# Kernel tuning notes

Measured on AMD Instinct MI355X. Metric: run time of the kernel, lower is better.

Reference implementation:

```python
import jax, jax.numpy as jnp
import numpy as np

NUM_HEADS = 8


def setup_inputs() -> dict:
    key = jax.random.key(0)
    ks = jax.random.split(key, 5)
    B, N, D = 2, 2048, 512
    scale = 1.0 / np.sqrt(D)  # xavier-ish init for stability
    return {
        "x": jax.random.normal(ks[0], (B, N, D), dtype=jnp.float32),
        "Wq": jax.random.normal(ks[1], (D, D), dtype=jnp.float32) * scale,
        "Wk": jax.random.normal(ks[2], (D, D), dtype=jnp.float32) * scale,
        "Wv": jax.random.normal(ks[3], (D, D), dtype=jnp.float32) * scale,
        "Wo": jax.random.normal(ks[4], (D, D), dtype=jnp.float32) * scale,
        "log_c": jnp.zeros((), dtype=jnp.float32),
        "log_beta": jnp.zeros((), dtype=jnp.float32),
    }


def reference(x, Wq, Wk, Wv, Wo, log_c, log_beta):
    B, N, D = x.shape
    H = NUM_HEADS
    dh = D // H

    # torch nn.Linear: y = x @ W.T
    def proj(W):
        return (x @ W.T).reshape(B, N, H, dh).transpose(0, 2, 1, 3)  # [B,H,N,dh]

    q, k, v = proj(Wq), proj(Wk), proj(Wv)

    c = jax.nn.softplus(log_c)
    beta = jax.nn.softplus(log_beta) + 0.5

    q_nsq = jnp.sum(q * q, axis=-1)  # [B,H,N]
    k_nsq = jnp.sum(k * k, axis=-1)  # [B,H,N]
    qk = jnp.einsum("bhnd,bhmd->bhnm", q, k)  # [B,H,N,N]

    diff_sq = jnp.maximum(q_nsq[..., :, None] - 2.0 * qk + k_nsq[..., None, :], 0.0)
    hyp_factor = jnp.sqrt(1.0 + c * (q_nsq[..., :, None] + k_nsq[..., None, :]))
    dist = jnp.sqrt(diff_sq + 1e-8) * hyp_factor
    scores = -beta * dist

    # causal mask (original: causal = mask is not None)
    causal = jnp.tril(jnp.ones((N, N), dtype=bool))
    scores = jnp.where(causal, scores, -jnp.inf)

    p = jax.nn.softmax(scores, axis=-1)
    out = jnp.einsum("bhnm,bhmd->bhnd", p, v)  # [B,H,N,dh]
    out = out.transpose(0, 2, 1, 3).reshape(B, N, D)
    return out @ Wo.T
```

## Files before the change

### kernel.cpp

```cpp
#include <hip/hip_runtime.h>
#include <math.h>

#define BB   2
#define NN   2048
#define DDIM 512
#define HH   8
#define DH   64
#define MTOT (BB*NN)
#define EE   (BB*HH*NN*DH)
#define CPB  144
#define NSLOT (BB*HH*CPB)

typedef __attribute__((ext_vector_type(8))) short bf16x8;
typedef __attribute__((ext_vector_type(4))) float f32x4;

__device__ __forceinline__ float softplus_f(float x) {
    return x > 20.f ? x : log1pf(expf(x));
}
__device__ __forceinline__ unsigned short f2bf(float x) {
    union { float f; unsigned u; } v; v.f = x;
    unsigned r = v.u + 0x7fffu + ((v.u >> 16) & 1u);
    return (unsigned short)(r >> 16);
}
__device__ __forceinline__ float bf2f(unsigned short h) {
    union { unsigned u; float f; } v; v.u = ((unsigned)h) << 16; return v.f;
}
__device__ __forceinline__ void split4(float4 v, ushort4& h, ushort4& l) {
    h.x = f2bf(v.x); l.x = f2bf(v.x - bf2f(h.x));
    h.y = f2bf(v.y); l.y = f2bf(v.y - bf2f(h.y));
    h.z = f2bf(v.z); l.z = f2bf(v.z - bf2f(h.z));
    h.w = f2bf(v.w); l.w = f2bf(v.w - bf2f(h.w));
}

template<int NT, bool PROJ>
__global__ __launch_bounds__(256, 3)
void mm_mfma(const float* __restrict__ Xf,
             const unsigned short* __restrict__ Ahg, const unsigned short* __restrict__ Alg,
             const float* __restrict__ W0, const float* __restrict__ W1,
             const float* __restrict__ W2,
             unsigned short* __restrict__ Qhi, unsigned short* __restrict__ Qlo,
             unsigned short* __restrict__ Khi, unsigned short* __restrict__ Klo,
             unsigned short* __restrict__ Vt, float* __restrict__ Outp,
             float* __restrict__ QN, float* __restrict__ KN)
{
    const int mode = PROJ ? (int)blockIdx.z : 3;
    const float* W = (mode == 1) ? W1 : ((mode == 2) ? W2 : W0);
    const int m0 = blockIdx.x * 64, n0 = blockIdx.y * NT;

    constexpr int NTT = NT / 32;
    constexpr int NW  = NT / 2;
    constexpr int KQS = NT * 8;

    __shared__ unsigned short Ah_s[4 * 64 * 8];
    __shared__ unsigned short Al_s[4 * 64 * 8];
    __shared__ unsigned short Bh_s[4 * NT * 8];
    __shared__ unsigned short Bl_s[4 * NT * 8];

    const int tid  = threadIdx.x;
    const int lane = tid & 63, lx = lane & 15, q4 = lane >> 4;
    const int w = tid >> 6, wm = w & 1, wn = w >> 1;
    const int rowA = tid & 63, kqA = tid >> 6;

    int rowB, kbB;
    if (NT == 128) { rowB = tid & 127; kbB = tid >> 7; }
    else           { rowB = tid & 63;  kbB = tid >> 6; }

    f32x4 acc[2][NTT];
    #pragma unroll
    for (int mt = 0; mt < 2; ++mt)
        #pragma unroll
        for (int nt = 0; nt < NTT; ++nt)
            acc[mt][nt] = (f32x4){0.f, 0.f, 0.f, 0.f};

    const int am = m0 + rowA;
    const int ab = am >> 11, an = am & 2047;
    const size_t brow = (size_t)(n0 + rowB) * DDIM;

    float4 fa0, fa1;
    uint4  rah, ral;
    float4 fb0, fb1, fb2, fb3;

    {
        const int e = kqA * 8;
        if (PROJ) {
            const float* ap = Xf + (size_t)am * DDIM + e;
            fa0 = *(const float4*)(ap);
            fa1 = *(const float4*)(ap + 4);
        } else {
            const size_t aoff = (((size_t)(ab * HH + (e >> 6)) * NN + an) << 6) + (e & 63);
            rah = *(const uint4*)(Ahg + aoff);
            ral = *(const uint4*)(Alg + aoff);
        }
        const int eb = kbB * 8;
        fb0 = *(const float4*)(W + brow + eb);
        fb1 = *(const float4*)(W + brow + eb + 4);
        if (NT == 128) {
            fb2 = *(const float4*)(W + brow + eb + 16);
            fb3 = *(const float4*)(W + brow + eb + 20);
        }
    }

    for (int k0 = 0; k0 < DDIM; k0 += 32) {
        __syncthreads();
        if (PROJ) {
            ushort4 h0, l0, h1, l1;
            split4(fa0, h0, l0); split4(fa1, h1, l1);
            const int off = (kqA << 9) + (rowA << 3);
            *(ushort4*)&Ah_s[off]     = h0;  *(ushort4*)&Ah_s[off + 4] = h1;
            *(ushort4*)&Al_s[off]     = l0;  *(ushort4*)&Al_s[off + 4] = l1;
        } else {
            const int off = (kqA << 9) + (rowA << 3);
            *(uint4*)&Ah_s[off] = rah;
            *(uint4*)&Al_s[off] = ral;
        }
        {
            ushort4 h0, l0, h1, l1;
            split4(fb0, h0, l0); split4(fb1, h1, l1);
            const int off = kbB * KQS + (rowB << 3);
            *(ushort4*)&Bh_s[off]     = h0;  *(ushort4*)&Bh_s[off + 4] = h1;
            *(ushort4*)&Bl_s[off]     = l0;  *(ushort4*)&Bl_s[off + 4] = l1;
            if (NT == 128) {
                split4(fb2, h0, l0); split4(fb3, h1, l1);
                const int off2 = (kbB + 2) * KQS + (rowB << 3);
                *(ushort4*)&Bh_s[off2]     = h0;  *(ushort4*)&Bh_s[off2 + 4] = h1;
                *(ushort4*)&Bl_s[off2]     = l0;  *(ushort4*)&Bl_s[off2 + 4] = l1;
            }
        }
        __syncthreads();

        if (k0 + 32 < DDIM) {
            const int e = k0 + 32 + kqA * 8;
            if (PROJ) {
                const float* ap = Xf + (size_t)am * DDIM + e;
                fa0 = *(const float4*)(ap);
                fa1 = *(const float4*)(ap + 4);
            } else {
                const size_t aoff = (((size_t)(ab * HH + (e >> 6)) * NN + an) << 6) + (e & 63);
                rah = *(const uint4*)(Ahg + aoff);
                ral = *(const uint4*)(Alg + aoff);
            }
            const int eb = k0 + 32 + kbB * 8;
            fb0 = *(const float4*)(W + brow + eb);
            fb1 = *(const float4*)(W + brow + eb + 4);
            if (NT == 128) {
                fb2 = *(const float4*)(W + brow + eb + 16);
                fb3 = *(const float4*)(W + brow + eb + 20);
            }
        }

        bf16x8 fah[2], fal[2], fbh[NTT], fbl[NTT];
        #pragma unroll
        for (int mt = 0; mt < 2; ++mt) {
            const int off = (q4 << 9) + ((wm * 32 + mt * 16 + lx) << 3);
            fah[mt] = *(const bf16x8*)&Ah_s[off];
            fal[mt] = *(const bf16x8*)&Al_s[off];
        }
        #pragma unroll
        for (int nt = 0; nt < NTT; ++nt) {
            const int off = q4 * KQS + ((wn * NW + nt * 16 + lx) << 3);
            fbh[nt] = *(const bf16x8*)&Bh_s[off];
            fbl[nt] = *(const bf16x8*)&Bl_s[off];
        }
        #pragma unroll
        for (int mt = 0; mt < 2; ++mt)
            #pragma unroll
            for (int nt = 0; nt < NTT; ++nt) {
                acc[mt][nt] = __builtin_amdgcn_mfma_f32_16x16x32_bf16(fah[mt], fbh[nt], acc[mt][nt], 0, 0, 0);
                acc[mt][nt] = __builtin_amdgcn_mfma_f32_16x16x32_bf16(fah[mt], fbl[nt], acc[mt][nt], 0, 0, 0);
                acc[mt][nt] = __builtin_amdgcn_mfma_f32_16x16x32_bf16(fal[mt], fbh[nt], acc[mt][nt], 0, 0, 0);
            }
    }

    if (PROJ && NT == 128 && (mode == 0 || mode == 1)) {
        float* Np = (mode == 0) ? QN : KN;
        const int head = (n0 + wn * 64) >> 6;
        #pragma unroll
        for (int mt = 0; mt < 2; ++mt)
            #pragma unroll
            for (int r = 0; r < 4; ++r) {
                float s = 0.f;
                #pragma unroll
                for (int nt = 0; nt < NTT; ++nt) s = fmaf(acc[mt][nt][r], acc[mt][nt][r], s);
                s += __shfl_xor(s, 1);
                s += __shfl_xor(s, 2);
                s += __shfl_xor(s, 4);
                s += __shfl_xor(s, 8);
                if (lx == 0) {
                    const int m = m0 + wm * 32 + mt * 16 + q4 * 4 + r;
                    Np[(size_t)((m >> 11) * HH + head) * NN + (m & 2047)] = s;
                }
            }
    }

    if (mode == 2) {
        #pragma unroll
        for (int mt = 0; mt < 2; ++mt) {
            const int mb = m0 + wm * 32 + mt * 16 + q4 * 4;
            const int b = mb >> 11, nb = mb & 2047;
            #pragma unroll
            for (int nt = 0; nt < NTT; ++nt) {
                const int j = n0 + wn * NW + nt * 16 + lx;
                ushort4 pv = make_ushort4(f2bf(acc[mt][nt][0]), f2bf(acc[mt][nt][1]),
                                          f2bf(acc[mt][nt][2]), f2bf(acc[mt][nt][3]));
                *(ushort4*)(Vt + ((size_t)(b * HH + (j >> 6)) * 64 + (j & 63)) * NN + nb) = pv;
            }
        }
    } else {
        #pragma unroll
        for (int mt = 0; mt < 2; ++mt) {
            #pragma unroll
            for (int r = 0; r < 4; ++r) {
                const int m = m0 + wm * 32 + mt * 16 + q4 * 4 + r;
                const int b = m >> 11, n2 = m & 2047;
                #pragma unroll
                for (int nt = 0; nt < NTT; ++nt) {
                    const int j = n0 + wn * NW + nt * 16 + lx;
                    const float v = acc[mt][nt][r];
                    if (mode == 3) {
                        Outp[(size_t)m * DDIM + j] = v;
                    } else {
                        const size_t idx = (((size_t)(b * HH + (j >> 6)) * NN + n2) << 6) + (j & 63);
                        const unsigned short h = f2bf(v);
                        const unsigned short l = f2bf(v - bf2f(h));
                        if (mode == 0) { Qhi[idx] = h; Qlo[idx] = l; }
                        else           { Khi[idx] = h; Klo[idx] = l; }
                    }
                }
            }
        }
    }
}

__global__ __launch_bounds__(256, 4)
void attn_mfma(const unsigned short* __restrict__ Qhi, const unsigned short* __restrict__ Qlo,
               const unsigned short* __restrict__ Khi, const unsigned short* __restrict__ Klo,
               const unsigned short* __restrict__ Vt,
               const float* __restrict__ QN, const float* __restrict__ KN,
               const float* __restrict__ pLC, const float* __restrict__ pLB,
               float* __restrict__ Opart, float* __restrict__ Mp, float* __restrict__ Lp)
{
    __shared__ unsigned short Kh_s[8 * 64 * 8];
    __shared__ unsigned short Kl_s[8 * 64 * 8];
    __shared__ unsigned short Vt_s[8 * 64 * 8];
    __shared__ unsigned short P_s [8 * 64 * 8];
    __shared__ float kn_s[64];
    __shared__ float qn_s[64];

    const int idx = blockIdx.x;
    const int g   = (idx >= 112) ? 7 : (idx >= 84) ? 6 : (idx >= 60) ? 5 :
                    (idx >= 40) ? 4 : (idx >= 24) ? 3 : (idx >= 12) ? 2 :
                    (idx >= 4)  ? 1 : 0;
    const int rem = idx - 2 * g * (g + 1);
    const int C   = g + 1;
    const int qt  = g * 4 + rem / C;
    const int c0  = rem % C;
    const int bh  = blockIdx.y;
    const int nk  = qt + 1;
    const int kt0  = (c0 * nk) / C;
    const int kend = ((c0 + 1) * nk) / C;

    const int tid  = threadIdx.x;
    const int w    = tid >> 6;
    const int lane = tid & 63;
    const int lx   = lane & 15;
    const int q4   = lane >> 4;

    const float hc    = softplus_f(pLC[0]);
    const float betaL = (softplus_f(pLB[0]) + 0.5f) * 1.44269504f;

    const size_t base = ((size_t)bh * NN) << 6;

    union { unsigned short u[8]; bf16x8 v; } ones_u;
    #pragma unroll
    for (int j = 0; j < 8; ++j) ones_u.u[j] = 0x3F80;
    const bf16x8 ones = ones_u.v;

    const unsigned short* qrh = Qhi + base + ((size_t)(qt * 64 + w * 16 + lx) << 6) + q4 * 8;
    const unsigned short* qrl = Qlo + base + ((size_t)(qt * 64 + w * 16 + lx) << 6) + q4 * 8;
    const bf16x8 qh0 = *(const bf16x8*)(qrh);
    const bf16x8 qh1 = *(const bf16x8*)(qrh + 32);
    const bf16x8 ql0 = *(const bf16x8*)(qrl);
    const bf16x8 ql1 = *(const bf16x8*)(qrl + 32);

    if (tid < 64) qn_s[tid] = QN[(size_t)bh * NN + qt * 64 + tid];

    f32x4 Oacc[4];
    f32x4 Lacc = (f32x4){0.f, 0.f, 0.f, 0.f};
    float m_st[4];
    #pragma unroll
    for (int r = 0; r < 4; ++r) {
        m_st[r] = -INFINITY;
        Oacc[r] = (f32x4){0.f, 0.f, 0.f, 0.f};
    }

    const int sc = tid >> 6, sr = tid & 63;

    uint4 pKh0, pKh1, pKl0, pKl1, pVt0, pVt1; float pkn = 0.f;
    {
        const unsigned short* kh = Khi + base + ((size_t)(kt0 * 64 + sr) << 6) + sc * 8;
        const unsigned short* kl = Klo + base + ((size_t)(kt0 * 64 + sr) << 6) + sc * 8;
        const unsigned short* vt = Vt  + base + (size_t)sr * NN + kt0 * 64 + sc * 8;
        pKh0 = *(const uint4*)(kh);  pKh1 = *(const uint4*)(kh + 32);
        pKl0 = *(const uint4*)(kl);  pKl1 = *(const uint4*)(kl + 32);
        pVt0 = *(const uint4*)(vt);  pVt1 = *(const uint4*)(vt + 32);
        if (tid < 64) pkn = KN[(size_t)bh * NN + kt0 * 64 + tid];
    }

    __syncthreads();

    for (int kt = kt0; kt < kend; ++kt) {
        const int soff = (sc << 9) + (sr << 3);
        *(uint4*)&Kh_s[soff]                = pKh0;
        *(uint4*)&Kh_s[soff + (4 << 9)]     = pKh1;
        *(uint4*)&Kl_s[soff]                = pKl0;
        *(uint4*)&Kl_s[soff + (4 << 9)]     = pKl1;
        *(uint4*)&Vt_s[soff]                = pVt0;
        *(uint4*)&Vt_s[soff + (4 << 9)]     = pVt1;
        if (tid < 64) kn_s[tid] = pkn;
        __syncthreads();

        if (kt + 1 < kend) {
            const unsigned short* kh = Khi + base + ((size_t)((kt + 1) * 64 + sr) << 6) + sc * 8;
            const unsigned short* kl = Klo + base + ((size_t)((kt + 1) * 64 + sr) << 6) + sc * 8;
            const unsigned short* vt = Vt  + base + (size_t)sr * NN + (kt + 1) * 64 + sc * 8;
            pKh0 = *(const uint4*)(kh);  pKh1 = *(const uint4*)(kh + 32);
            pKl0 = *(const uint4*)(kl);  pKl1 = *(const uint4*)(kl + 32);
            pVt0 = *(const uint4*)(vt);  pVt1 = *(const uint4*)(vt + 32);
            if (tid < 64) pkn = KN[(size_t)bh * NN + (kt + 1) * 64 + tid];
        }

        f32x4 S[4];
        #pragma unroll
        for (int t = 0; t < 4; ++t) {
            f32x4 acc = (f32x4){0.f, 0.f, 0.f, 0.f};
            #pragma unroll
            for (int c2 = 0; c2 < 2; ++c2) {
                const int off = ((c2 * 4 + q4) << 9) + (t << 7) + (lx << 3);
                const bf16x8 kh = *(const bf16x8*)&Kh_s[off];
                const bf16x8 kl = *(const bf16x8*)&Kl_s[off];
                const bf16x8 qh = c2 ? qh1 : qh0;
                const bf16x8 ql = c2 ? ql1 : ql0;
                acc = __builtin_amdgcn_mfma_f32_16x16x32_bf16(qh, kh, acc, 0, 0, 0);
                acc = __builtin_amdgcn_mfma_f32_16x16x32_bf16(qh, kl, acc, 0, 0, 0);
                acc = __builtin_amdgcn_mfma_f32_16x16x32_bf16(ql, kh, acc, 0, 0, 0);
            }
            S[t] = acc;
        }

        float qn_r[4];
        #pragma unroll
        for (int r = 0; r < 4; ++r) qn_r[r] = qn_s[w * 16 + q4 * 4 + r];
        const bool diag = (kt == qt);

        float mrow[4] = {-INFINITY, -INFINITY, -INFINITY, -INFINITY};
        #pragma unroll
        for (int t = 0; t < 4; ++t) {
            const float kn = kn_s[t * 16 + lx];
            #pragma unroll
            for (int r = 0; r < 4; ++r) {
                const float sumn = qn_r[r] + kn;
                float diff = fmaxf(fmaf(-2.f, S[t][r], sumn), 0.f);
                float s = -betaL * sqrtf(fmaf(hc, sumn, 1.f) * (diff + 1e-8f));
                const int cc = t * 16 + lx;
                const int rr = w * 16 + q4 * 4 + r;
                if (diag && cc > rr) s = -INFINITY;
                S[t][r] = s;
                mrow[r] = fmaxf(mrow[r], s);
            }
        }

        #pragma unroll
        for (int r = 0; r < 4; ++r) {
            float m = mrow[r];
            m = fmaxf(m, __shfl_xor(m, 1));
            m = fmaxf(m, __shfl_xor(m, 2));
            m = fmaxf(m, __shfl_xor(m, 4));
            m = fmaxf(m, __shfl_xor(m, 8));
            const float mn = fmaxf(m_st[r], m);
            const float al = exp2f(m_st[r] - mn);
            m_st[r] = mn;
            const int prow = ((w * 16 + q4 * 4 + r) << 3) + (lx & 7);
            #pragma unroll
            for (int t = 0; t < 4; ++t) {
                const float p = exp2f(S[t][r] - mn);
                P_s[((t * 2 + (lx >> 3)) << 9) + prow] = f2bf(p);
                Oacc[t][r] *= al;
            }
            Lacc[r] *= al;
        }

        __builtin_amdgcn_wave_barrier();

        #pragma unroll
        for (int c2 = 0; c2 < 2; ++c2) {
            const bf16x8 pa = *(const bf16x8*)&P_s[((c2 * 4 + q4) << 9) + ((w * 16 + lx) << 3)];
            #pragma unroll
            for (int t = 0; t < 4; ++t) {
                const bf16x8 vb = *(const bf16x8*)&Vt_s[((c2 * 4 + q4) << 9) + (t << 7) + (lx << 3)];
                Oacc[t] = __builtin_amdgcn_mfma_f32_16x16x32_bf16(pa, vb, Oacc[t], 0, 0, 0);
            }
            Lacc = __builtin_amdgcn_mfma_f32_16x16x32_bf16(pa, ones, Lacc, 0, 0, 0);
        }
        __syncthreads();
    }

    const int slot = bh * CPB + idx;
    float* op = Opart + ((size_t)slot << 12);
    #pragma unroll
    for (int r = 0; r < 4; ++r) {
        const int row = w * 16 + q4 * 4 + r;
        #pragma unroll
        for (int t = 0; t < 4; ++t)
            op[row * 64 + t * 16 + lx] = Oacc[t][r];
        if (lx == 0) {
            Mp[slot * 64 + row] = m_st[r];
            Lp[slot * 64 + row] = Lacc[r];
        }
    }
}

__global__ __launch_bounds__(256)
void attn_combine(const float* __restrict__ Opart, const float* __restrict__ Mp,
                  const float* __restrict__ Lp,
                  unsigned short* __restrict__ AOh, unsigned short* __restrict__ AOl)
{
    const int bh = blockIdx.x >> 5, qt = blockIdx.x & 31;
    const int g = qt >> 2, C = g + 1;
    const int first = 2 * g * (g + 1) + (qt & 3) * C;
    const int row = threadIdx.x >> 2, qd = threadIdx.x & 3;
    const int slot0 = bh * CPB + first;

    float m = -INFINITY;
    for (int c = 0; c < C; ++c) m = fmaxf(m, Mp[(slot0 + c) * 64 + row]);
    float L = 0.f;
    float o[16];
    #pragma unroll
    for (int j = 0; j < 16; ++j) o[j] = 0.f;

    for (int c = 0; c < C; ++c) {
        const float wgt = exp2f(Mp[(slot0 + c) * 64 + row] - m);
        L += wgt * Lp[(slot0 + c) * 64 + row];
        const float* op = Opart + (((size_t)(slot0 + c)) << 12) + row * 64 + qd * 16;
        #pragma unroll
        for (int j4 = 0; j4 < 4; ++j4) {
            float4 v = *(const float4*)(op + j4 * 4);
            o[j4*4+0] = fmaf(wgt, v.x, o[j4*4+0]);
            o[j4*4+1] = fmaf(wgt, v.y, o[j4*4+1]);
            o[j4*4+2] = fmaf(wgt, v.z, o[j4*4+2]);
            o[j4*4+3] = fmaf(wgt, v.w, o[j4*4+3]);
        }
    }

    const float inv = 1.f / L;
    const size_t obase = (((size_t)bh * NN + qt * 64 + row) << 6) + qd * 16;
    union { unsigned short u[8]; uint4 v; } h2[2], l2[2];
    #pragma unroll
    for (int j = 0; j < 16; ++j) {
        const float ov = o[j] * inv;
        const unsigned short h = f2bf(ov);
        const unsigned short l = f2bf(ov - bf2f(h));
        h2[j >> 3].u[j & 7] = h;
        l2[j >> 3].u[j & 7] = l;
    }
    *(uint4*)(AOh + obase)     = h2[0].v;
    *(uint4*)(AOh + obase + 8) = h2[1].v;
    *(uint4*)(AOl + obase)     = l2[0].v;
    *(uint4*)(AOl + obase + 8) = l2[1].v;
}

extern "C" void kernel_launch(void* const* d_in, const int* in_sizes, int n_in,
                              void* d_out, int out_size, void* d_ws, size_t ws_size,
                              hipStream_t stream)
{
    const float* x        = (const float*)d_in[0];
    const float* Wq       = (const float*)d_in[1];
    const float* Wk       = (const float*)d_in[2];
    const float* Wv       = (const float*)d_in[3];
    const float* Wo       = (const float*)d_in[4];
    const float* log_c    = (const float*)d_in[5];
    const float* log_beta = (const float*)d_in[6];
    float* out = (float*)d_out;

    unsigned short* p = (unsigned short*)d_ws;
    unsigned short* Qhi = p;            p += EE;
    unsigned short* Qlo = p;            p += EE;
    unsigned short* Khi = p;            p += EE;
    unsigned short* Klo = p;            p += EE;
    unsigned short* Vtr = p;            p += EE;
    unsigned short* AOh = p;            p += EE;
    unsigned short* AOl = p;            p += EE;
    float* QN    = (float*)p;
    float* KN    = QN + (size_t)BB * HH * NN;
    float* Opart = KN + (size_t)BB * HH * NN;
    float* Mp    = Opart + (size_t)NSLOT * 64 * 64;
    float* Lp    = Mp + (size_t)NSLOT * 64;

    mm_mfma<128, true><<<dim3(MTOT / 64, DDIM / 128, 3), 256, 0, stream>>>(
        x, nullptr, nullptr, Wq, Wk, Wv,
        Qhi, Qlo, Khi, Klo, Vtr, nullptr, QN, KN);
    attn_mfma<<<dim3(CPB, 16), 256, 0, stream>>>(Qhi, Qlo, Khi, Klo, Vtr, QN, KN,
                                                 log_c, log_beta, Opart, Mp, Lp);
    attn_combine<<<dim3(512), 256, 0, stream>>>(Opart, Mp, Lp, AOh, AOl);
    mm_mfma<64, false><<<dim3(MTOT / 64, DDIM / 64, 1), 256, 0, stream>>>(
        nullptr, AOh, AOl, Wo, nullptr, nullptr,
        nullptr, nullptr, nullptr, nullptr, nullptr, out, nullptr, nullptr);
}
```

Measured before the change: 206.6 us.

## Use single bf16 for output projection and transpose attention MFMA layout

```diff
diff --git a/kernel.cpp b/kernel.cpp
--- a/kernel.cpp
+++ b/kernel.cpp
@@ -32,123 +32,83 @@
     h.w = f2bf(v.w); l.w = f2bf(v.w - bf2f(h.w));
 }
 
-template<int NT, bool PROJ>
 __global__ __launch_bounds__(256, 3)
-void mm_mfma(const float* __restrict__ Xf,
-             const unsigned short* __restrict__ Ahg, const unsigned short* __restrict__ Alg,
+void mm_proj(const float* __restrict__ Xf,
              const float* __restrict__ W0, const float* __restrict__ W1,
              const float* __restrict__ W2,
              unsigned short* __restrict__ Qhi, unsigned short* __restrict__ Qlo,
              unsigned short* __restrict__ Khi, unsigned short* __restrict__ Klo,
-             unsigned short* __restrict__ Vt, float* __restrict__ Outp,
+             unsigned short* __restrict__ Vt,
              float* __restrict__ QN, float* __restrict__ KN)
 {
-    const int mode = PROJ ? (int)blockIdx.z : 3;
+    const int mode = blockIdx.z;
     const float* W = (mode == 1) ? W1 : ((mode == 2) ? W2 : W0);
-    const int m0 = blockIdx.x * 64, n0 = blockIdx.y * NT;
-
-    constexpr int NTT = NT / 32;
-    constexpr int NW  = NT / 2;
-    constexpr int KQS = NT * 8;
+    const int m0 = blockIdx.x * 64, n0 = blockIdx.y * 128;
 
     __shared__ unsigned short Ah_s[4 * 64 * 8];
     __shared__ unsigned short Al_s[4 * 64 * 8];
-    __shared__ unsigned short Bh_s[4 * NT * 8];
-    __shared__ unsigned short Bl_s[4 * NT * 8];
+    __shared__ unsigned short Bh_s[4 * 128 * 8];
+    __shared__ unsigned short Bl_s[4 * 128 * 8];
 
     const int tid  = threadIdx.x;
     const int lane = tid & 63, lx = lane & 15, q4 = lane >> 4;
     const int w = tid >> 6, wm = w & 1, wn = w >> 1;
     const int rowA = tid & 63, kqA = tid >> 6;
-
-    int rowB, kbB;
-    if (NT == 128) { rowB = tid & 127; kbB = tid >> 7; }
-    else           { rowB = tid & 63;  kbB = tid >> 6; }
-
-    f32x4 acc[2][NTT];
+    const int rowB = tid & 127, kbB = tid >> 7;
+
+    f32x4 acc[2][4];
     #pragma unroll
     for (int mt = 0; mt < 2; ++mt)
         #pragma unroll
-        for (int nt = 0; nt < NTT; ++nt)
+        for (int nt = 0; nt < 4; ++nt)
             acc[mt][nt] = (f32x4){0.f, 0.f, 0.f, 0.f};
 
     const int am = m0 + rowA;
-    const int ab = am >> 11, an = am & 2047;
     const size_t brow = (size_t)(n0 + rowB) * DDIM;
 
-    float4 fa0, fa1;
-    uint4  rah, ral;
-    float4 fb0, fb1, fb2, fb3;
-
+    float4 fa0, fa1, fb0, fb1, fb2, fb3;
     {
-        const int e = kqA * 8;
-        if (PROJ) {
-            const float* ap = Xf + (size_t)am * DDIM + e;
-            fa0 = *(const float4*)(ap);
-            fa1 = *(const float4*)(ap + 4);
-        } else {
-            const size_t aoff = (((size_t)(ab * HH + (e >> 6)) * NN + an) << 6) + (e & 63);
-            rah = *(const uint4*)(Ahg + aoff);
-            ral = *(const uint4*)(Alg + aoff);
-        }
+        const float* ap = Xf + (size_t)am * DDIM + kqA * 8;
+        fa0 = *(const float4*)(ap);
+        fa1 = *(const float4*)(ap + 4);
         const int eb = kbB * 8;
         fb0 = *(const float4*)(W + brow + eb);
         fb1 = *(const float4*)(W + brow + eb + 4);
-        if (NT == 128) {
-            fb2 = *(const float4*)(W + brow + eb + 16);
-            fb3 = *(const float4*)(W + brow + eb + 20);
-        }
+        fb2 = *(const float4*)(W + brow + eb + 16);
+        fb3 = *(const float4*)(W + brow + eb + 20);
     }
 
     for (int k0 = 0; k0 < DDIM; k0 += 32) {
         __syncthreads();
-        if (PROJ) {
+        {
             ushort4 h0, l0, h1, l1;
             split4(fa0, h0, l0); split4(fa1, h1, l1);
             const int off = (kqA << 9) + (rowA << 3);
             *(ushort4*)&Ah_s[off]     = h0;  *(ushort4*)&Ah_s[off + 4] = h1;
             *(ushort4*)&Al_s[off]     = l0;  *(ushort4*)&Al_s[off + 4] = l1;
-        } else {
-            const int off = (kqA << 9) + (rowA << 3);
-            *(uint4*)&Ah_s[off] = rah;
-            *(uint4*)&Al_s[off] = ral;
-        }
-        {
-            ushort4 h0, l0, h1, l1;
             split4(fb0, h0, l0); split4(fb1, h1, l1);
-            const int off = kbB * KQS + (rowB << 3);
-            *(ushort4*)&Bh_s[off]     = h0;  *(ushort4*)&Bh_s[off + 4] = h1;
-            *(ushort4*)&Bl_s[off]     = l0;  *(ushort4*)&Bl_s[off + 4] = l1;
-            if (NT == 128) {
-                split4(fb2, h0, l0); split4(fb3, h1, l1);
-                const int off2 = (kbB + 2) * KQS + (rowB << 3);
-                *(ushort4*)&Bh_s[off2]     = h0;  *(ushort4*)&Bh_s[off2 + 4] = h1;
-                *(ushort4*)&Bl_s[off2]     = l0;  *(ushort4*)&Bl_s[off2 + 4] = l1;
-            }
+            const int offb = (kbB << 10) + (rowB << 3);
+            *(ushort4*)&Bh_s[offb]     = h0;  *(ushort4*)&Bh_s[offb + 4] = h1;
+            *(ushort4*)&Bl_s[offb]     = l0;  *(ushort4*)&Bl_s[offb + 4] = l1;
+            split4(fb2, h0, l0); split4(fb3, h1, l1);
+            const int offb2 = ((kbB + 2) << 10) + (rowB << 3);
+            *(ushort4*)&Bh_s[offb2]     = h0;  *(ushort4*)&Bh_s[offb2 + 4] = h1;
+            *(ushort4*)&Bl_s[offb2]     = l0;  *(ushort4*)&Bl_s[offb2 + 4] = l1;
         }
         __syncthreads();
 
         if (k0 + 32 < DDIM) {
-            const int e = k0 + 32 + kqA * 8;
-            if (PROJ) {
-                const float* ap = Xf + (size_t)am * DDIM + e;
-                fa0 = *(const float4*)(ap);
-                fa1 = *(const float4*)(ap + 4);
-            } else {
-                const size_t aoff = (((size_t)(ab * HH + (e >> 6)) * NN + an) << 6) + (e & 63);
-                rah = *(const uint4*)(Ahg + aoff);
-                ral = *(const uint4*)(Alg + aoff);
-            }
+            const float* ap = Xf + (size_t)am * DDIM + k0 + 32 + kqA * 8;
+            fa0 = *(const float4*)(ap);
+            fa1 = *(const float4*)(ap + 4);
             const int eb = k0 + 32 + kbB * 8;
             fb0 = *(const float4*)(W + brow + eb);
             fb1 = *(const float4*)(W + brow + eb + 4);
-            if (NT == 128) {
-                fb2 = *(const float4*)(W + brow + eb + 16);
-                fb3 = *(const float4*)(W + brow + eb + 20);
-            }
-        }
-
-        bf16x8 fah[2], fal[2], fbh[NTT], fbl[NTT];
+            fb2 = *(const float4*)(W + brow + eb + 16);
+            fb3 = *(const float4*)(W + brow + eb + 20);
+        }
+
+        bf16x8 fah[2], fal[2], fbh[4], fbl[4];
         #pragma unroll
         for (int mt = 0; mt < 2; ++mt) {
             const int off = (q4 << 9) + ((wm * 32 + mt * 16 + lx) << 3);
@@ -156,22 +116,22 @@
             fal[mt] = *(const bf16x8*)&Al_s[off];
         }
         #pragma unroll
-        for (int nt = 0; nt < NTT; ++nt) {
-            const int off = q4 * KQS + ((wn * NW + nt * 16 + lx) << 3);
+        for (int nt = 0; nt < 4; ++nt) {
+            const int off = (q4 << 10) + ((wn * 64 + nt * 16 + lx) << 3);
             fbh[nt] = *(const bf16x8*)&Bh_s[off];
             fbl[nt] = *(const bf16x8*)&Bl_s[off];
         }
         #pragma unroll
         for (int mt = 0; mt < 2; ++mt)
             #pragma unroll
-            for (int nt = 0; nt < NTT; ++nt) {
+            for (int nt = 0; nt < 4; ++nt) {
                 acc[mt][nt] = __builtin_amdgcn_mfma_f32_16x16x32_bf16(fah[mt], fbh[nt], acc[mt][nt], 0, 0, 0);
                 acc[mt][nt] = __builtin_amdgcn_mfma_f32_16x16x32_bf16(fah[mt], fbl[nt], acc[mt][nt], 0, 0, 0);
                 acc[mt][nt] = __builtin_amdgcn_mfma_f32_16x16x32_bf16(fal[mt], fbh[nt], acc[mt][nt], 0, 0, 0);
             }
     }
 
-    if (PROJ && NT == 128 && (mode == 0 || mode == 1)) {
+    if (mode == 0 || mode == 1) {
         float* Np = (mode == 0) ? QN : KN;
         const int head = (n0 + wn * 64) >> 6;
         #pragma unroll
@@ -180,7 +140,7 @@
             for (int r = 0; r < 4; ++r) {
                 float s = 0.f;
                 #pragma unroll
-                for (int nt = 0; nt < NTT; ++nt) s = fmaf(acc[mt][nt][r], acc[mt][nt][r], s);
+                for (int nt = 0; nt < 4; ++nt) s = fmaf(acc[mt][nt][r], acc[mt][nt][r], s);
                 s += __shfl_xor(s, 1);
                 s += __shfl_xor(s, 2);
                 s += __shfl_xor(s, 4);
@@ -198,8 +158,8 @@
             const int mb = m0 + wm * 32 + mt * 16 + q4 * 4;
             const int b = mb >> 11, nb = mb & 2047;
             #pragma unroll
-            for (int nt = 0; nt < NTT; ++nt) {
-                const int j = n0 + wn * NW + nt * 16 + lx;
+            for (int nt = 0; nt < 4; ++nt) {
+                const int j = n0 + wn * 64 + nt * 16 + lx;
                 ushort4 pv = make_ushort4(f2bf(acc[mt][nt][0]), f2bf(acc[mt][nt][1]),
                                           f2bf(acc[mt][nt][2]), f2bf(acc[mt][nt][3]));
                 *(ushort4*)(Vt + ((size_t)(b * HH + (j >> 6)) * 64 + (j & 63)) * NN + nb) = pv;
@@ -213,22 +173,95 @@
                 const int m = m0 + wm * 32 + mt * 16 + q4 * 4 + r;
                 const int b = m >> 11, n2 = m & 2047;
                 #pragma unroll
-                for (int nt = 0; nt < NTT; ++nt) {
-                    const int j = n0 + wn * NW + nt * 16 + lx;
+                for (int nt = 0; nt < 4; ++nt) {
+                    const int j = n0 + wn * 64 + nt * 16 + lx;
                     const float v = acc[mt][nt][r];
-                    if (mode == 3) {
-                        Outp[(size_t)m * DDIM + j] = v;
-                    } else {
-                        const size_t idx = (((size_t)(b * HH + (j >> 6)) * NN + n2) << 6) + (j & 63);
-                        const unsigned short h = f2bf(v);
-                        const unsigned short l = f2bf(v - bf2f(h));
-                        if (mode == 0) { Qhi[idx] = h; Qlo[idx] = l; }
-                        else           { Khi[idx] = h; Klo[idx] = l; }
-                    }
+                    const size_t idx = (((size_t)(b * HH + (j >> 6)) * NN + n2) << 6) + (j & 63);
+                    const unsigned short h = f2bf(v);
+                    const unsigned short l = f2bf(v - bf2f(h));
+                    if (mode == 0) { Qhi[idx] = h; Qlo[idx] = l; }
+                    else           { Khi[idx] = h; Klo[idx] = l; }
                 }
             }
         }
     }
+}
+
+__global__ __launch_bounds__(256, 4)
+void mm_out(const unsigned short* __restrict__ AO, const float* __restrict__ Wo,
+            float* __restrict__ Outp)
+{
+    const int m0 = blockIdx.x * 64, n0 = blockIdx.y * 64;
+
+    __shared__ unsigned short Ah_s[4 * 64 * 8];
+    __shared__ unsigned short Bh_s[4 * 64 * 8];
+
+    const int tid  = threadIdx.x;
+    const int lane = tid & 63, lx = lane & 15, q4 = lane >> 4;
+    const int w = tid >> 6, wm = w & 1, wn = w >> 1;
+    const int rowA = tid & 63, kqA = tid >> 6;
+
+    f32x4 acc[2][2];
+    #pragma unroll
+    for (int mt = 0; mt < 2; ++mt)
+        #pragma unroll
+        for (int nt = 0; nt < 2; ++nt)
+            acc[mt][nt] = (f32x4){0.f, 0.f, 0.f, 0.f};
+
+    const int am = m0 + rowA;
+    const int ab = am >> 11, an = am & 2047;
+    const size_t brow = (size_t)(n0 + rowA) * DDIM;
+
+    uint4 rah; float4 fb0, fb1;
+    {
+        const int e = kqA * 8;
+        rah = *(const uint4*)(AO + (((size_t)(ab * HH + (e >> 6)) * NN + an) << 6) + (e & 63));
+        fb0 = *(const float4*)(Wo + brow + e);
+        fb1 = *(const float4*)(Wo + brow + e + 4);
+    }
+
+    for (int k0 = 0; k0 < DDIM; k0 += 32) {
+        __syncthreads();
+        {
+            const int off = (kqA << 9) + (rowA << 3);
+            *(uint4*)&Ah_s[off] = rah;
+            ushort4 h0 = make_ushort4(f2bf(fb0.x), f2bf(fb0.y), f2bf(fb0.z), f2bf(fb0.w));
+            ushort4 h1 = make_ushort4(f2bf(fb1.x), f2bf(fb1.y), f2bf(fb1.z), f2bf(fb1.w));
+            *(ushort4*)&Bh_s[off]     = h0;
+            *(ushort4*)&Bh_s[off + 4] = h1;
+        }
+        __syncthreads();
+
+        if (k0 + 32 < DDIM) {
+            const int e = k0 + 32 + kqA * 8;
+            rah = *(const uint4*)(AO + (((size_t)(ab * HH + (e >> 6)) * NN + an) << 6) + (e & 63));
+            fb0 = *(const float4*)(Wo + brow + e);
+            fb1 = *(const float4*)(Wo + brow + e + 4);
+        }
+
+        bf16x8 fah[2], fbh[2];
+        #pragma unroll
+        for (int mt = 0; mt < 2; ++mt)
+            fah[mt] = *(const bf16x8*)&Ah_s[(q4 << 9) + ((wm * 32 + mt * 16 + lx) << 3)];
+        #pragma unroll
+        for (int nt = 0; nt < 2; ++nt)
+            fbh[nt] = *(const bf16x8*)&Bh_s[(q4 << 9) + ((wn * 32 + nt * 16 + lx) << 3)];
+        #pragma unroll
+        for (int mt = 0; mt < 2; ++mt)
+            #pragma unroll
+            for (int nt = 0; nt < 2; ++nt)
+                acc[mt][nt] = __builtin_amdgcn_mfma_f32_16x16x32_bf16(fah[mt], fbh[nt], acc[mt][nt], 0, 0, 0);
+    }
+
+    #pragma unroll
+    for (int mt = 0; mt < 2; ++mt)
+        #pragma unroll
+        for (int r = 0; r < 4; ++r) {
+            const int m = m0 + wm * 32 + mt * 16 + q4 * 4 + r;
+            #pragma unroll
+            for (int nt = 0; nt < 2; ++nt)
+                Outp[(size_t)m * DDIM + n0 + wn * 32 + nt * 16 + lx] = acc[mt][nt][r];
+        }
 }
 
 __global__ __launch_bounds__(256, 4)
@@ -243,7 +276,7 @@
     __shared__ unsigned short Kl_s[8 * 64 * 8];
     __shared__ unsigned short Vt_s[8 * 64 * 8];
     __shared__ unsigned short P_s [8 * 64 * 8];
-    __shared__ float kn_s[64];
+    __shared__ __align__(16) float kn_s[64];
     __shared__ float qn_s[64];
 
     const int idx = blockIdx.x;
@@ -264,34 +297,26 @@
     const int lane = tid & 63;
     const int lx   = lane & 15;
     const int q4   = lane >> 4;
+    const int qrl  = w * 16 + lx;
 
     const float hc    = softplus_f(pLC[0]);
     const float betaL = (softplus_f(pLB[0]) + 0.5f) * 1.44269504f;
 
     const size_t base = ((size_t)bh * NN) << 6;
 
-    union { unsigned short u[8]; bf16x8 v; } ones_u;
-    #pragma unroll
-    for (int j = 0; j < 8; ++j) ones_u.u[j] = 0x3F80;
-    const bf16x8 ones = ones_u.v;
-
-    const unsigned short* qrh = Qhi + base + ((size_t)(qt * 64 + w * 16 + lx) << 6) + q4 * 8;
-    const unsigned short* qrl = Qlo + base + ((size_t)(qt * 64 + w * 16 + lx) << 6) + q4 * 8;
+    const unsigned short* qrh = Qhi + base + ((size_t)(qt * 64 + qrl) << 6) + q4 * 8;
+    const unsigned short* qrl_p = Qlo + base + ((size_t)(qt * 64 + qrl) << 6) + q4 * 8;
     const bf16x8 qh0 = *(const bf16x8*)(qrh);
     const bf16x8 qh1 = *(const bf16x8*)(qrh + 32);
-    const bf16x8 ql0 = *(const bf16x8*)(qrl);
-    const bf16x8 ql1 = *(const bf16x8*)(qrl + 32);
+    const bf16x8 ql0 = *(const bf16x8*)(qrl_p);
+    const bf16x8 ql1 = *(const bf16x8*)(qrl_p + 32);
 
     if (tid < 64) qn_s[tid] = QN[(size_t)bh * NN + qt * 64 + tid];
 
     f32x4 Oacc[4];
-    f32x4 Lacc = (f32x4){0.f, 0.f, 0.f, 0.f};
-    float m_st[4];
-    #pragma unroll
-    for (int r = 0; r < 4; ++r) {
-        m_st[r] = -INFINITY;
-        Oacc[r] = (f32x4){0.f, 0.f, 0.f, 0.f};
-    }
+    #pragma unroll
+    for (int t = 0; t < 4; ++t) Oacc[t] = (f32x4){0.f, 0.f, 0.f, 0.f};
+    float m_st = -INFINITY, l_st = 0.f;
 
     const int sc = tid >> 6, sr = tid & 63;
 
@@ -307,15 +332,16 @@
     }
 
     __syncthreads();
+    const float qn = qn_s[qrl];
 
     for (int kt = kt0; kt < kend; ++kt) {
         const int soff = (sc << 9) + (sr << 3);
-        *(uint4*)&Kh_s[soff]                = pKh0;
-        *(uint4*)&Kh_s[soff + (4 << 9)]     = pKh1;
-        *(uint4*)&Kl_s[soff]                = pKl0;
-        *(uint4*)&Kl_s[soff + (4 << 9)]     = pKl1;
-        *(uint4*)&Vt_s[soff]                = pVt0;
-        *(uint4*)&Vt_s[soff + (4 << 9)]     = pVt1;
+        *(uint4*)&Kh_s[soff]            = pKh0;
+        *(uint4*)&Kh_s[soff + (4 << 9)] = pKh1;
+        *(uint4*)&Kl_s[soff]            = pKl0;
+        *(uint4*)&Kl_s[soff + (4 << 9)] = pKl1;
+        *(uint4*)&Vt_s[soff]            = pVt0;
+        *(uint4*)&Vt_s[soff + (4 << 9)] = pVt1;
         if (tid < 64) kn_s[tid] = pkn;
         __syncthreads();
 
@@ -335,71 +361,70 @@
             f32x4 acc = (f32x4){0.f, 0.f, 0.f, 0.f};
             #pragma unroll
             for (int c2 = 0; c2 < 2; ++c2) {
-                const int off = ((c2 * 4 + q4) << 9) + (t << 7) + (lx << 3);
+                const int off = ((c2 * 4 + q4) << 9) + ((t * 16 + lx) << 3);
                 const bf16x8 kh = *(const bf16x8*)&Kh_s[off];
                 const bf16x8 kl = *(const bf16x8*)&Kl_s[off];
                 const bf16x8 qh = c2 ? qh1 : qh0;
                 const bf16x8 ql = c2 ? ql1 : ql0;
-                acc = __builtin_amdgcn_mfma_f32_16x16x32_bf16(qh, kh, acc, 0, 0, 0);
-                acc = __builtin_amdgcn_mfma_f32_16x16x32_bf16(qh, kl, acc, 0, 0, 0);
-                acc = __builtin_amdgcn_mfma_f32_16x16x32_bf16(ql, kh, acc, 0, 0, 0);
+                acc = __builtin_amdgcn_mfma_f32_16x16x32_bf16(kh, qh, acc, 0, 0, 0);
+                acc = __builtin_amdgcn_mfma_f32_16x16x32_bf16(kh, ql, acc, 0, 0, 0);
+                acc = __builtin_amdgcn_mfma_f32_16x16x32_bf16(kl, qh, acc, 0, 0, 0);
             }
             S[t] = acc;
         }
 
-        float qn_r[4];
-        #pragma unroll
-        for (int r = 0; r < 4; ++r) qn_r[r] = qn_s[w * 16 + q4 * 4 + r];
         const bool diag = (kt == qt);
-
-        float mrow[4] = {-INFINITY, -INFINITY, -INFINITY, -INFINITY};
+        float mloc = -INFINITY;
         #pragma unroll
         for (int t = 0; t < 4; ++t) {
-            const float kn = kn_s[t * 16 + lx];
+            float kn4[4];
+            *(float4*)kn4 = *(const float4*)&kn_s[t * 16 + q4 * 4];
             #pragma unroll
             for (int r = 0; r < 4; ++r) {
-                const float sumn = qn_r[r] + kn;
+                const float sumn = qn + kn4[r];
                 float diff = fmaxf(fmaf(-2.f, S[t][r], sumn), 0.f);
                 float s = -betaL * sqrtf(fmaf(hc, sumn, 1.f) * (diff + 1e-8f));
-                const int cc = t * 16 + lx;
-                const int rr = w * 16 + q4 * 4 + r;
-                if (diag && cc > rr) s = -INFINITY;
+                if (diag && (t * 16 + q4 * 4 + r) > qrl) s = -INFINITY;
                 S[t][r] = s;
-                mrow[r] = fmaxf(mrow[r], s);
-            }
-        }
-
-        #pragma unroll
-        for (int r = 0; r < 4; ++r) {
-            float m = mrow[r];
-            m = fmaxf(m, __shfl_xor(m, 1));
-            m = fmaxf(m, __shfl_xor(m, 2));
-            m = fmaxf(m, __shfl_xor(m, 4));
-            m = fmaxf(m, __shfl_xor(m, 8));
-            const float mn = fmaxf(m_st[r], m);
-            const float al = exp2f(m_st[r] - mn);
-            m_st[r] = mn;
-            const int prow = ((w * 16 + q4 * 4 + r) << 3) + (lx & 7);
-            #pragma unroll
-            for (int t = 0; t < 4; ++t) {
-                const float p = exp2f(S[t][r] - mn);
-                P_s[((t * 2 + (lx >> 3)) << 9) + prow] = f2bf(p);
-                Oacc[t][r] *= al;
-            }
-            Lacc[r] *= al;
+                mloc = fmaxf(mloc, s);
+            }
+        }
+        mloc = fmaxf(mloc, __shfl_xor(mloc, 16));
+        mloc = fmaxf(mloc, __shfl_xor(mloc, 32));
+        const float mn = fmaxf(m_st, mloc);
+        const float al = exp2f(m_st - mn);
+        m_st = mn;
+
+        float rs = 0.f;
+        #pragma unroll
+        for (int t = 0; t < 4; ++t) {
+            const float p0 = exp2f(S[t][0] - mn);
+            const float p1 = exp2f(S[t][1] - mn);
+            const float p2 = exp2f(S[t][2] - mn);
+            const float p3 = exp2f(S[t][3] - mn);
+            rs += (p0 + p1) + (p2 + p3);
+            ushort4 pk = make_ushort4(f2bf(p0), f2bf(p1), f2bf(p2), f2bf(p3));
+            *(ushort4*)&P_s[((2 * t + (q4 >> 1)) << 9) + (qrl << 3) + ((q4 & 1) << 2)] = pk;
+        }
+        rs += __shfl_xor(rs, 16);
+        rs += __shfl_xor(rs, 32);
+        l_st = l_st * al + rs;
+        #pragma unroll
+        for (int t = 0; t < 4; ++t) {
+            Oacc[t][0] *= al; Oacc[t][1] *= al;
+            Oacc[t][2] *= al; Oacc[t][3] *= al;
         }
 
         __builtin_amdgcn_wave_barrier();
 
         #pragma unroll
         for (int c2 = 0; c2 < 2; ++c2) {
-            const bf16x8 pa = *(const bf16x8*)&P_s[((c2 * 4 + q4) << 9) + ((w * 16 + lx) << 3)];
-            #pragma unroll
-            for (int t = 0; t < 4; ++t) {
-                const bf16x8 vb = *(const bf16x8*)&Vt_s[((c2 * 4 + q4) << 9) + (t << 7) + (lx << 3)];
-                Oacc[t] = __builtin_amdgcn_mfma_f32_16x16x32_bf16(pa, vb, Oacc[t], 0, 0, 0);
-            }
-            Lacc = __builtin_amdgcn_mfma_f32_16x16x32_bf16(pa, ones, Lacc, 0, 0, 0);
+            const bf16x8 pb = *(const bf16x8*)&P_s[((c2 * 4 + q4) << 9) + (qrl << 3)];
+            #pragma unroll
+            for (int t2 = 0; t2 < 4; ++t2) {
+                const bf16x8 va = *(const bf16x8*)&Vt_s[((c2 * 4 + q4) << 9) + ((t2 * 16 + lx) << 3)];
+                Oacc[t2] = __builtin_amdgcn_mfma_f32_16x16x32_bf16(va, pb, Oacc[t2], 0, 0, 0);
+            }
         }
         __syncthreads();
     }
@@ -407,22 +432,17 @@
     const int slot = bh * CPB + idx;
     float* op = Opart + ((size_t)slot << 12);
     #pragma unroll
-    for (int r = 0; r < 4; ++r) {
-        const int row = w * 16 + q4 * 4 + r;
-        #pragma unroll
-        for (int t = 0; t < 4; ++t)
-            op[row * 64 + t * 16 + lx] = Oacc[t][r];
-        if (lx == 0) {
-            Mp[slot * 64 + row] = m_st[r];
-            Lp[slot * 64 + row] = Lacc[r];
-        }
+    for (int t2 = 0; t2 < 4; ++t2)
+        *(f32x4*)&op[qrl * 64 + t2 * 16 + q4 * 4] = Oacc[t2];
+    if (q4 == 0) {
+        Mp[slot * 64 + qrl] = m_st;
+        Lp[slot * 64 + qrl] = l_st;
     }
 }
 
 __global__ __launch_bounds__(256)
 void attn_combine(const float* __restrict__ Opart, const float* __restrict__ Mp,
-                  const float* __restrict__ Lp,
-                  unsigned short* __restrict__ AOh, unsigned short* __restrict__ AOl)
+                  const float* __restrict__ Lp, unsigned short* __restrict__ AO)
 {
     const int bh = blockIdx.x >> 5, qt = blockIdx.x & 31;
     const int g = qt >> 2, C = g + 1;
@@ -453,19 +473,12 @@
 
     const float inv = 1.f / L;
     const size_t obase = (((size_t)bh * NN + qt * 64 + row) << 6) + qd * 16;
-    union { unsigned short u[8]; uint4 v; } h2[2], l2[2];
-    #pragma unroll
-    for (int j = 0; j < 16; ++j) {
-        const float ov = o[j] * inv;
-        const unsigned short h = f2bf(ov);
-        const unsigned short l = f2bf(ov - bf2f(h));
-        h2[j >> 3].u[j & 7] = h;
-        l2[j >> 3].u[j & 7] = l;
-    }
-    *(uint4*)(AOh + obase)     = h2[0].v;
-    *(uint4*)(AOh + obase + 8) = h2[1].v;
-    *(uint4*)(AOl + obase)     = l2[0].v;
-    *(uint4*)(AOl + obase + 8) = l2[1].v;
+    union { unsigned short u[8]; uint4 v; } h2[2];
+    #pragma unroll
+    for (int j = 0; j < 16; ++j)
+        h2[j >> 3].u[j & 7] = f2bf(o[j] * inv);
+    *(uint4*)(AO + obase)     = h2[0].v;
+    *(uint4*)(AO + obase + 8) = h2[1].v;
 }
 
 extern "C" void kernel_launch(void* const* d_in, const int* in_sizes, int n_in,
@@ -487,21 +500,17 @@
     unsigned short* Khi = p;            p += EE;
     unsigned short* Klo = p;            p += EE;
     unsigned short* Vtr = p;            p += EE;
-    unsigned short* AOh = p;            p += EE;
-    unsigned short* AOl = p;            p += EE;
+    unsigned short* AO  = p;            p += EE;
     float* QN    = (float*)p;
     float* KN    = QN + (size_t)BB * HH * NN;
     float* Opart = KN + (size_t)BB * HH * NN;
     float* Mp    = Opart + (size_t)NSLOT * 64 * 64;
     float* Lp    = Mp + (size_t)NSLOT * 64;
 
-    mm_mfma<128, true><<<dim3(MTOT / 64, DDIM / 128, 3), 256, 0, stream>>>(
-        x, nullptr, nullptr, Wq, Wk, Wv,
-        Qhi, Qlo, Khi, Klo, Vtr, nullptr, QN, KN);
+    mm_proj<<<dim3(MTOT / 64, DDIM / 128, 3), 256, 0, stream>>>(
+        x, Wq, Wk, Wv, Qhi, Qlo, Khi, Klo, Vtr, QN, KN);
     attn_mfma<<<dim3(CPB, 16), 256, 0, stream>>>(Qhi, Qlo, Khi, Klo, Vtr, QN, KN,
                                                  log_c, log_beta, Opart, Mp, Lp);
-    attn_combine<<<dim3(512), 256, 0, stream>>>(Opart, Mp, Lp, AOh, AOl);
-    mm_mfma<64, false><<<dim3(MTOT / 64, DDIM / 64, 1), 256, 0, stream>>>(
-        nullptr, AOh, AOl, Wo, nullptr, nullptr,
-        nullptr, nullptr, nullptr, nullptr, nullptr, out, nullptr, nullptr);
-}
+    attn_combine<<<dim3(512), 256, 0, stream>>>(Opart, Mp, Lp, AO);
+    mm_out<<<dim3(MTOT / 64, DDIM / 64), 256, 0, stream>>>(AO, Wo, out);
+}
```

New measurement: 190.5 us. 7.8% less time.
